# Optimization experiments

Measured on AMD Instinct MI355X. Metric: run time of the kernel, lower is better.

## Reference

```python
import jax, jax.numpy as jnp
import numpy as np
from jax import lax

B, S, I, H, O, L = 32, 512, 256, 1024, 256, 3


def setup_inputs() -> dict:
    key = jax.random.key(0)
    ks = jax.random.split(key, 10)
    sc = 0.02
    return {
        "x": jax.random.normal(ks[0], (B, S, I), dtype=jnp.float32),
        "h0": jnp.zeros((B, L, H), dtype=jnp.float32),
        # layer 0 params: gates ordered [z, r, g]
        "Wx0": jax.random.normal(ks[1], (3, H, I), dtype=jnp.float32) * sc,
        "Wh0": jax.random.normal(ks[2], (3, H, H), dtype=jnp.float32) * sc,
        "bh0": jax.random.normal(ks[3], (3, H), dtype=jnp.float32) * sc,
        # layers 1..L-1 params (input dim = H)
        "Wx": jax.random.normal(ks[4], (L - 1, 3, H, H), dtype=jnp.float32) * sc,
        "Wh": jax.random.normal(ks[5], (L - 1, 3, H, H), dtype=jnp.float32) * sc,
        "bh": jax.random.normal(ks[6], (L - 1, 3, H), dtype=jnp.float32) * sc,
        "Wout": jax.random.normal(ks[7], (O, H), dtype=jnp.float32) * sc,
        "bout": jax.random.normal(ks[8], (O,), dtype=jnp.float32) * sc,
    }


def _gru_layer(x_seq, h0, Wx, Wh, bh):
    # x_seq: [S,B,Iin], h0: [B,H], Wx: [3,H,Iin], Wh: [3,H,H], bh: [3,H]
    # Precompute all input projections once (fused GEMM over full sequence).
    xproj = jnp.einsum('sbi,ghi->sbgh', x_seq, Wx)  # [S,B,3,H]

    def step(h, xp):
        z = jax.nn.sigmoid(xp[:, 0] + h @ Wh[0].T + bh[0])
        r = jax.nn.sigmoid(xp[:, 1] + h @ Wh[1].T + bh[1])
        g = jnp.tanh(xp[:, 2] + (r * h) @ Wh[2].T + bh[2])
        h_new = z * h + (1.0 - z) * g
        return h_new, h_new

    h_last, hs = lax.scan(step, h0, xproj)
    return hs, h_last  # hs: [S,B,H]


def reference(x, h0, Wx0, Wh0, bh0, Wx, Wh, bh, Wout, bout):
    seq = jnp.transpose(x, (1, 0, 2))  # [S,B,I]
    cur, hl = _gru_layer(seq, h0[:, 0], Wx0, Wh0, bh0)
    finals = [hl]
    n_extra = Wx.shape[0]
    for i in range(n_extra):  # small fixed layer count
        cur, hl = _gru_layer(cur, h0[:, i + 1], Wx[i], Wh[i], bh[i])
        finals.append(hl)
    out = cur @ Wout.T + bout  # [S,B,O]
    layer_output = jnp.transpose(out, (1, 0, 2))  # [B,S,O]
    hidden_state = jnp.stack(finals, axis=1)  # [B,L,H]
    return layer_output, hidden_state
```

## Files before the change

### kernel.cpp

```cpp
#include <hip/hip_runtime.h>
#include <cstdint>
#include <cstddef>

#define S_  512
#define H_  1024
#define H3  3072
#define OUT_OFF 4194304

typedef __attribute__((ext_vector_type(8))) short  short8;
typedef __attribute__((ext_vector_type(4))) float  f32x4;
typedef __attribute__((ext_vector_type(4))) unsigned short us4;
typedef __attribute__((ext_vector_type(4))) unsigned int   u32x4;
typedef unsigned long long u64;

#define MFMA __builtin_amdgcn_mfma_f32_16x16x32_bf16

static const size_t XP_OFF    = 0;
static const size_t H2_OFF    = 100663296;
static const size_t XBF_OFF   = 134217728;
static const size_t WX0B_OFF  = 142606336;
static const size_t WZR0_OFF  = 144179200;
static const size_t WG0_OFF   = 148373504;
static const size_t WZR1_OFF  = 150470656;
static const size_t WGX1_OFF  = 158859264;
static const size_t WG1_OFF   = 160956416;
static const size_t WZR2_OFF  = 163053568;
static const size_t WGX2_OFF  = 171442176;
static const size_t WG2_OFF   = 173539328;
static const size_t WOUTB_OFF = 175636480;
static const size_t ZBU_OFF   = 176160768;
static const size_t GXB_OFF   = 176553984;
static const size_t HROW_OFF  = 176947200;
static const size_t FLAG_OFF  = 177340416;
static const size_t HH_OFF    = 177344512;
static const size_t RHH_OFF   = 278597632;
static const size_t WS_HIST   = 379654144;
static const size_t WS_BASE   = 177737728;

__device__ inline unsigned short f2bf(float f){
  unsigned u = __builtin_bit_cast(unsigned, f);
  unsigned r = u + 0x7fffu + ((u >> 16) & 1u);
  return (unsigned short)(r >> 16);
}
__device__ inline float bf2f(unsigned short s){
  unsigned u = ((unsigned)s) << 16;
  return __builtin_bit_cast(float, u);
}
__device__ inline unsigned ld_sys(const unsigned* p){
  return __hip_atomic_load(p, __ATOMIC_RELAXED, __HIP_MEMORY_SCOPE_AGENT);
}
__device__ inline void st_sys(unsigned* p, unsigned v){
  __hip_atomic_store(p, v, __ATOMIC_RELAXED, __HIP_MEMORY_SCOPE_AGENT);
}
__device__ inline u64 ld64(const u64* p){
  return __hip_atomic_load(p, __ATOMIC_RELAXED, __HIP_MEMORY_SCOPE_AGENT);
}
__device__ inline void st64(u64* p, u64 v){
  __hip_atomic_store(p, v, __ATOMIC_RELAXED, __HIP_MEMORY_SCOPE_AGENT);
}
template<bool HIST>
__device__ inline u64 LD(const u64* p){
  if constexpr (HIST) return *p; else return ld64(p);
}
__device__ inline short8 mk8u(u64 a, u64 b){
  u32x4 u; u.x = (unsigned)a; u.y = (unsigned)(a >> 32); u.z = (unsigned)b; u.w = (unsigned)(b >> 32);
  return __builtin_bit_cast(short8, u);
}
__device__ inline u64 pk4(float a, float b, float c, float d){
  return (u64)f2bf(a) | ((u64)f2bf(b) << 16) | ((u64)f2bf(c) << 32) | ((u64)f2bf(d) << 48);
}
__device__ inline u64 pk2f(float a, float b){
  return (u64)__builtin_bit_cast(unsigned, a) | ((u64)__builtin_bit_cast(unsigned, b) << 32);
}
__device__ inline float lo32f(u64 u){ return __builtin_bit_cast(float, (unsigned)u); }
__device__ inline float hi32f(u64 u){ return __builtin_bit_cast(float, (unsigned)(u >> 32)); }

__global__ void k_conv(const float* __restrict__ src, unsigned short* __restrict__ dst, int n){
  int i = blockIdx.x*256 + threadIdx.x;
  if (i < n) dst[i] = f2bf(src[i]);
}
__global__ void k_packzr(const float* __restrict__ Wh, const float* __restrict__ Wx,
                         unsigned short* __restrict__ dst){
  size_t i = (size_t)blockIdx.x*256 + threadIdx.x;
  int k = (int)(i & 2047);
  int n = (int)(i >> 11);
  float v = (k < 1024) ? Wh[(size_t)n*1024 + k] : Wx[(size_t)n*1024 + (k - 1024)];
  dst[i] = f2bf(v);
}
__global__ void k_convx(const float* __restrict__ x, unsigned short* __restrict__ xbf){
  int row = blockIdx.x;
  int s = row >> 5, b = row & 31;
  int i = threadIdx.x;
  xbf[(size_t)row*256 + i] = f2bf(x[((size_t)b*S_ + s)*256 + i]);
}

__global__ __launch_bounds__(256) void k_gemm(const unsigned short* __restrict__ A,
                                              const unsigned short* __restrict__ Bw,
                                              const float* __restrict__ bias,
                                              void* __restrict__ Cout,
                                              int Kd, int mode, int Nd){
  __shared__ __align__(16) unsigned short lA[128*40];
  __shared__ __align__(16) unsigned short lB[128*40];
  int bm = blockIdx.y * 128, bn = blockIdx.x * 128;
  int tid = threadIdx.x;
  int w = tid >> 6, lane = tid & 63, q = lane >> 4, cc = lane & 15;
  int wm = (w >> 1) * 64, wn = (w & 1) * 64;
  f32x4 acc[4][4] = {};
  for (int k0 = 0; k0 < Kd; k0 += 32){
    #pragma unroll
    for (int i = 0; i < 2; i++){
      int idx = tid + i*256;
      int r = idx >> 2, ch = idx & 3;
      int m = bm + r;
      int arow = (mode == 0) ? m : ((m & 511)*32 + (m >> 9));
      *(u32x4*)(lA + r*40 + ch*8) = *(const u32x4*)(A + (size_t)arow*Kd + k0 + ch*8);
      *(u32x4*)(lB + r*40 + ch*8) = *(const u32x4*)(Bw + (size_t)(bn + r)*Kd + k0 + ch*8);
    }
    __syncthreads();
    short8 af[4], bfv[4];
    #pragma unroll
    for (int i = 0; i < 4; i++) af[i]  = *(const short8*)(lA + (wm + i*16 + cc)*40 + q*8);
    #pragma unroll
    for (int i = 0; i < 4; i++) bfv[i] = *(const short8*)(lB + (wn + i*16 + cc)*40 + q*8);
    #pragma unroll
    for (int i = 0; i < 4; i++)
      #pragma unroll
      for (int j = 0; j < 4; j++)
        acc[i][j] = MFMA(af[i], bfv[j], acc[i][j], 0, 0, 0);
    __syncthreads();
  }
  if (mode == 0){
    unsigned short* xp = (unsigned short*)Cout;
    #pragma unroll
    for (int i = 0; i < 4; i++){
      #pragma unroll
      for (int j = 0; j < 4; j++){
        int m = bm + wm + i*16 + q*4;
        int n = bn + wn + j*16 + cc;
        float bv = bias[n];
        int s = m >> 5, b0 = m & 31;
        us4 pk;
        #pragma unroll
        for (int reg = 0; reg < 4; reg++) pk[reg] = f2bf(acc[i][j][reg] + bv);
        *(us4*)(xp + ((size_t)s*H3 + n)*32 + b0) = pk;
      }
    }
  } else {
    float* C = (float*)Cout;
    #pragma unroll
    for (int i = 0; i < 4; i++){
      #pragma unroll
      for (int j = 0; j < 4; j++){
        int m = bm + wm + i*16 + q*4;
        int n = bn + wn + j*16 + cc;
        float bv = bias[n];
        #pragma unroll
        for (int reg = 0; reg < 4; reg++)
          C[(size_t)(m + reg)*Nd + n] = acc[i][j][reg] + bv;
      }
    }
  }
}

__device__ inline void gbar(unsigned* flags, unsigned ep){
  __syncthreads();
  if (threadIdx.x == 0) st_sys(flags + blockIdx.x, ep);
  if (threadIdx.x < 64){
    for (;;){
      unsigned v0 = ld_sys(flags + threadIdx.x);
      unsigned v1 = ld_sys(flags + 64 + threadIdx.x);
      unsigned v2 = ld_sys(flags + 128 + threadIdx.x);
      unsigned v3 = ld_sys(flags + 192 + threadIdx.x);
      if (__all((v0 >= ep) && (v1 >= ep) && (v2 >= ep) && (v3 >= ep))) break;
      __builtin_amdgcn_s_sleep(1);
    }
  }
  __syncthreads();
}

__device__ inline void waitflags(const unsigned* f, int lo, int hi, unsigned ep){
  if (threadIdx.x < 64){
    const unsigned* p = f + lo + threadIdx.x;
    const int n = hi - lo;
    const bool h1 = (n > 64), h2 = (n > 128);
    for (;;){
      unsigned v0 = ld_sys(p);
      unsigned v1 = h1 ? ld_sys(p + 64)  : 0xffffffffu;
      unsigned v2 = h2 ? ld_sys(p + 128) : 0xffffffffu;
      if (__all((v0 >= ep) && (v1 >= ep) && (v2 >= ep))) break;
      __builtin_amdgcn_s_sleep(1);
    }
  }
  __syncthreads();
}

template<int NITER, bool HIST>
__device__ inline void matvec(const u64* p0, const unsigned short* wp,
                              f32x4& acc0, f32x4& acc1){
  u64 buf[2][4][4];
  #pragma unroll
  for (int ii = 0; ii < 4; ii++){
    const u64* p = p0 + ii*256;
    buf[0][ii][0] = LD<HIST>(p);      buf[0][ii][1] = LD<HIST>(p + 32);
    buf[0][ii][2] = LD<HIST>(p + 16); buf[0][ii][3] = LD<HIST>(p + 48);
  }
  constexpr int NCH = NITER / 4;
  #pragma unroll
  for (int ch = 0; ch < NCH; ch++){
    const int cur = ch & 1, nxt = cur ^ 1;
    if (ch + 1 < NCH){
      #pragma unroll
      for (int ii = 0; ii < 4; ii++){
        const u64* p = p0 + ((ch+1)*4 + ii)*256;
        buf[nxt][ii][0] = LD<HIST>(p);      buf[nxt][ii][1] = LD<HIST>(p + 32);
        buf[nxt][ii][2] = LD<HIST>(p + 16); buf[nxt][ii][3] = LD<HIST>(p + 48);
      }
    }
    #pragma unroll
    for (int ii = 0; ii < 4; ii++){
      short8 bw = *(const short8*)(wp + (ch*4 + ii)*32);
      acc0 = MFMA(mk8u(buf[cur][ii][0], buf[cur][ii][1]), bw, acc0, 0, 0, 0);
      acc1 = MFMA(mk8u(buf[cur][ii][2], buf[cur][ii][3]), bw, acc1, 0, 0, 0);
    }
  }
}

template<int MODE>
__global__ __launch_bounds__(256, 1) void k_fused(char* __restrict__ ws,
                                                  const float* __restrict__ h0,
                                                  const float* __restrict__ bh,
                                                  float* __restrict__ outp,
                                                  u64* __restrict__ hh,
                                                  u64* __restrict__ rhh){
  constexpr bool HIST = (MODE >= 1);
  constexpr bool DF   = (MODE == 2);

  __shared__ __align__(16) unsigned short wlds[65920];
  __shared__ __align__(16) float red[2][3][64][10];
  __shared__ float rtA[16*33];
  __shared__ float rtB[16*33];

  const int tid = threadIdx.x;
  const int w = tid >> 6, lane = tid & 63, q = (lane >> 4) & 3, c = lane & 15;
  const int i = blockIdx.x;

  const int lz   = 1 + (i >> 7);
  const int g2   = (i >> 6) & 1;
  const int n2   = (i & 63) << 4;
  const bool isl0 = (i < 128);
  const int g1   = (i >> 6) & 1;
  const int lgx  = 1 + ((i >> 6) & 1);
  const int n1   = (i & 63) << 4;
  const bool hasB = (i < 192);
  const int lb   = i >> 6;
  const int nb   = (i & 63) << 4;

  const int alo = (lb == 2) ? 128 : 0;
  const int ahi = (lb == 0) ? 128 : (lb == 1 ? 192 : 256);

  const unsigned short* xp = (const unsigned short*)(ws + XP_OFF);
  u64* h2u   = (u64*)(ws + H2_OFF);
  u64* zbu   = (u64*)(ws + ZBU_OFF);
  u64* gxb   = (u64*)(ws + GXB_OFF);
  float* hrow = (float*)(ws + HROW_OFF);
  unsigned* flags = (unsigned*)(ws + FLAG_OFF);
  unsigned* flagA = flags + 256;
  unsigned* flagB = flags + 512;

  {
    const unsigned short* src2 = (const unsigned short*)(ws + (lz == 1 ? WZR1_OFF : WZR2_OFF))
                                 + (size_t)(g2*1024 + n2)*2048;
    for (int idx = tid; idx < 4096; idx += 256){
      int kc = idx & 255, row = idx >> 8;
      u32x4 v = *(const u32x4*)(src2 + (size_t)row*2048 + kc*8);
      *(u32x4*)(wlds + row*2056 + kc*8) = v;
    }
    const unsigned short* src1 = isl0
      ? (const unsigned short*)(ws + WZR0_OFF) + (size_t)(g1*1024 + n1)*1024
      : (const unsigned short*)(ws + (lgx == 1 ? WGX1_OFF : WGX2_OFF)) + (size_t)n1*1024;
    for (int idx = tid; idx < 2048; idx += 256){
      int kc = idx & 127, row = idx >> 7;
      u32x4 v = *(const u32x4*)(src1 + (size_t)row*1024 + kc*8);
      *(u32x4*)(wlds + 32896 + row*1032 + kc*8) = v;
    }
    if (hasB){
      const unsigned short* srcb = (const unsigned short*)(ws + (lb == 0 ? WG0_OFF : (lb == 1 ? WG1_OFF : WG2_OFF)))
                                   + (size_t)nb*1024;
      for (int idx = tid; idx < 2048; idx += 256){
        int kc = idx & 127, row = idx >> 7;
        u32x4 v = *(const u32x4*)(srcb + (size_t)row*1024 + kc*8);
        *(u32x4*)(wlds + 49408 + row*1032 + kc*8) = v;
      }
    }
  }
  const float biasT2 = bh[(size_t)(lz-1)*H3 + g2*1024 + n2 + c];
  const float biasGX = isl0 ? 0.f : bh[(size_t)(lgx-1)*H3 + 2048 + n1 + c];

  if (hasB){
    for (int idx = tid; idx < 512; idx += 256){
      int n = idx >> 5, b = idx & 31;
      float v = h0[((size_t)b*3 + lb)*H_ + nb + n];
      hrow[((size_t)lb*1024 + nb + n)*32 + b] = v;
      rtA[n*33 + b] = v;
    }
  }
  __syncthreads();
  if (hasB && tid < 128){
    int b = tid & 31, p2 = tid >> 5;
    u64 pkv = pk4(rtA[(4*p2+0)*33+b], rtA[(4*p2+1)*33+b], rtA[(4*p2+2)*33+b], rtA[(4*p2+3)*33+b]);
    st64(hh + (size_t)(HIST ? lb : 0)*24576 + (size_t)lb*8192 + (size_t)((nb >> 2) + p2)*32 + b, pkv);
  }
  unsigned ep = 1;
  if constexpr (DF){
    __syncthreads();
    if (tid == 0 && hasB) st_sys(flagB + i, (unsigned)(lb + 1));
  } else {
    gbar(flags, ep); ep++;
  }

  for (int T = 0; T < 514; T++){
    const int t2 = T - lz;
    const bool actT2 = (unsigned)t2 < 512u;
    const int t1 = isl0 ? T : (T - lgx);
    const bool actT1 = (unsigned)t1 < 512u;
    const int tb = T - lb;
    const bool actB = hasB && ((unsigned)tb < 512u);

    const u64* hslotR = hh + (size_t)(HIST ? T : 0)*24576;
    u64*       rslot  = rhh + (size_t)(HIST ? T : 0)*24576;

    if constexpr (DF){
      int lo = 256, hi = 0;
      if (actT2){ int a = 64*(lz-1), b = 64*(lz+1); if (a < lo) lo = a; if (b > hi) hi = b; }
      if (actT1){
        int a = isl0 ? 0 : 64*(lgx-1);
        int b = isl0 ? 64 : 64*(lgx+1);
        if (a < lo) lo = a; if (b > hi) hi = b;
      }
      if (hi > lo) waitflags(flagB, lo, hi, (unsigned)(T + 1));
    }

    u64 hpreA[8]; us4 xpreA[2]; u64 hpreL0[8];
    if (actT2 && w == 0 && g2 == 1){
      const u64* hb = hslotR + (size_t)lz*8192 + (size_t)((n2 + c) >> 2)*32 + q*4;
      #pragma unroll
      for (int mt = 0; mt < 2; mt++)
        #pragma unroll
        for (int r = 0; r < 4; r++) hpreA[mt*4+r] = LD<HIST>(hb + mt*16 + r);
    }
    if (actT1 && w == 1 && isl0){
      const unsigned short* xr = xp + ((size_t)t1*H3 + g1*1024 + n1 + c)*32 + q*4;
      xpreA[0] = *(const us4*)(xr);
      xpreA[1] = *(const us4*)(xr + 16);
      if (g1 == 1){
        const u64* hb = hslotR + (size_t)((n1 + c) >> 2)*32 + q*4;
        #pragma unroll
        for (int mt = 0; mt < 2; mt++)
          #pragma unroll
          for (int r = 0; r < 4; r++) hpreL0[mt*4+r] = LD<HIST>(hb + mt*16 + r);
      }
    }

    f32x4 z20 = {0,0,0,0}, z21 = {0,0,0,0};
    f32x4 z10 = {0,0,0,0}, z11 = {0,0,0,0};
    if (actT2){
      const u64* p0 = hslotR + (size_t)((w < 2) ? lz : (lz-1))*8192 + (size_t)((w & 1)*128 + q*2)*32 + c;
      const unsigned short* wp = wlds + c*2056 + w*512 + q*8;
      matvec<16, HIST>(p0, wp, z20, z21);
    }
    if (actT1){
      const u64* p0 = hslotR + (size_t)(isl0 ? 0 : (lgx-1))*8192 + (size_t)(w*64 + q*2)*32 + c;
      const unsigned short* wp = wlds + 32896 + c*1032 + w*256 + q*8;
      matvec<8, HIST>(p0, wp, z10, z11);
    }
    if (actT2 && w > 0){
      float* p = &red[0][w-1][lane][0];
      #pragma unroll
      for (int r = 0; r < 4; r++){ p[r] = z20[r]; p[4+r] = z21[r]; }
    }
    if (actT1 && w != 1){
      float* p = &red[1][(w == 0) ? 0 : (w-1)][lane][0];
      #pragma unroll
      for (int r = 0; r < 4; r++){ p[r] = z10[r]; p[4+r] = z11[r]; }
    }
    __syncthreads();
    if (w == 0 && actT2){
      #pragma unroll
      for (int s = 0; s < 3; s++){
        const float* p = &red[0][s][lane][0];
        #pragma unroll
        for (int r = 0; r < 4; r++){ z20[r] += p[r]; z21[r] += p[4+r]; }
      }
      const int sh = (c & 3)*16;
      #pragma unroll
      for (int mt = 0; mt < 2; mt++){
        float f[4];
        #pragma unroll
        for (int r = 0; r < 4; r++){
          float pre = (mt ? z21[r] : z20[r]) + biasT2;
          f[r] = 1.0f / (1.0f + __expf(-pre));
        }
        if (g2 == 0){
          u64* zp = zbu + ((size_t)lz*1024 + n2 + c)*16 + mt*8 + q*2;
          st64(zp, pk2f(f[0], f[1])); st64(zp + 1, pk2f(f[2], f[3]));
        } else {
          #pragma unroll
          for (int r = 0; r < 4; r++){
            int b = mt*16 + q*4 + r;
            rtA[c*33 + b] = f[r] * bf2f((unsigned short)(hpreA[mt*4+r] >> sh));
          }
        }
      }
    }
    if (w == 1 && actT1){
      #pragma unroll
      for (int s = 0; s < 3; s++){
        const float* p = &red[1][s][lane][0];
        #pragma unroll
        for (int r = 0; r < 4; r++){ z10[r] += p[r]; z11[r] += p[4+r]; }
      }
      if (isl0){
        const int sh = (c & 3)*16;
        #pragma unroll
        for (int mt = 0; mt < 2; mt++){
          us4 xv = xpreA[mt];
          float f[4];
          #pragma unroll
          for (int r = 0; r < 4; r++){
            float pre = (mt ? z11[r] : z10[r]) + bf2f(xv[r]);
            f[r] = 1.0f / (1.0f + __expf(-pre));
          }
          if (g1 == 0){
            u64* zp = zbu + ((size_t)n1 + c)*16 + mt*8 + q*2;
            st64(zp, pk2f(f[0], f[1])); st64(zp + 1, pk2f(f[2], f[3]));
          } else {
            #pragma unroll
            for (int r = 0; r < 4; r++){
              int b = mt*16 + q*4 + r;
              rtB[c*33 + b] = f[r] * bf2f((unsigned short)(hpreL0[mt*4+r] >> sh));
            }
          }
        }
      } else {
        #pragma unroll
        for (int mt = 0; mt < 2; mt++){
          float f[4];
          #pragma unroll
          for (int r = 0; r < 4; r++) f[r] = (mt ? z11[r] : z10[r]) + biasGX;
          u64* gp = gxb + ((size_t)lgx*1024 + n1 + c)*16 + mt*8 + q*2;
          st64(gp, pk2f(f[0], f[1])); st64(gp + 1, pk2f(f[2], f[3]));
        }
      }
    }
    __syncthreads();
    if (g2 == 1 && actT2 && tid < 128){
      int b = tid & 31, p2 = tid >> 5;
      st64(rslot + (size_t)lz*8192 + (size_t)((n2 >> 2) + p2)*32 + b,
           pk4(rtA[(4*p2+0)*33+b], rtA[(4*p2+1)*33+b], rtA[(4*p2+2)*33+b], rtA[(4*p2+3)*33+b]));
    }
    if (isl0 && g1 == 1 && actT1 && tid >= 128){
      int tt = tid - 128; int b = tt & 31, p2 = tt >> 5;
      st64(rslot + (size_t)((n1 >> 2) + p2)*32 + b,
           pk4(rtB[(4*p2+0)*33+b], rtB[(4*p2+1)*33+b], rtB[(4*p2+2)*33+b], rtB[(4*p2+3)*33+b]));
    }
    if constexpr (DF){
      __syncthreads();
      if (tid == 0 && (actT2 || actT1)) st_sys(flagA + i, (unsigned)(T + 1));
      if (actB) waitflags(flagA, alo, ahi, (unsigned)(T + 1));
    } else {
      gbar(flags, ep); ep++;
    }

    u64 zpreB[4], gpreB[4]; us4 xpreB[2]; f32x4 hpre4[2];
    if (actB && w == 0){
      const u64* zp = zbu + ((size_t)lb*1024 + nb + c)*16 + q*2;
      zpreB[0] = ld64(zp);     zpreB[1] = ld64(zp + 1);
      zpreB[2] = ld64(zp + 8); zpreB[3] = ld64(zp + 9);
      if (lb == 0){
        const unsigned short* xr = xp + ((size_t)tb*H3 + 2048 + nb + c)*32 + q*4;
        xpreB[0] = *(const us4*)(xr);
        xpreB[1] = *(const us4*)(xr + 16);
      } else {
        const u64* gp = gxb + ((size_t)lb*1024 + nb + c)*16 + q*2;
        gpreB[0] = ld64(gp);     gpreB[1] = ld64(gp + 1);
        gpreB[2] = ld64(gp + 8); gpreB[3] = ld64(gp + 9);
      }
      const float* hp0 = hrow + ((size_t)lb*1024 + nb + c)*32 + q*4;
      hpre4[0] = *(const f32x4*)(hp0);
      hpre4[1] = *(const f32x4*)(hp0 + 16);
    }

    f32x4 gb0 = {0,0,0,0}, gb1 = {0,0,0,0};
    if (actB){
      const u64* p0 = (const u64*)rslot + (size_t)lb*8192 + (size_t)(w*64 + q*2)*32 + c;
      const unsigned short* wp = wlds + 49408 + c*1032 + w*256 + q*8;
      matvec<8, HIST>(p0, wp, gb0, gb1);
      if (w > 0){
        float* p = &red[0][w-1][lane][0];
        #pragma unroll
        for (int r = 0; r < 4; r++){ p[r] = gb0[r]; p[4+r] = gb1[r]; }
      }
    }
    __syncthreads();
    if (actB && w == 0){
      #pragma unroll
      for (int s = 0; s < 3; s++){
        const float* p = &red[0][s][lane][0];
        #pragma unroll
        for (int r = 0; r < 4; r++){ gb0[r] += p[r]; gb1[r] += p[4+r]; }
      }
      #pragma unroll
      for (int mt = 0; mt < 2; mt++){
        float gadd[4];
        if (lb == 0){
          us4 xv = xpreB[mt];
          #pragma unroll
          for (int r = 0; r < 4; r++) gadd[r] = bf2f(xv[r]);
        } else {
          gadd[0] = lo32f(gpreB[mt*2]);   gadd[1] = hi32f(gpreB[mt*2]);
          gadd[2] = lo32f(gpreB[mt*2+1]); gadd[3] = hi32f(gpreB[mt*2+1]);
        }
        float zf[4] = { lo32f(zpreB[mt*2]),   hi32f(zpreB[mt*2]),
                        lo32f(zpreB[mt*2+1]), hi32f(zpreB[mt*2+1]) };
        f32x4 h4 = hpre4[mt];
        f32x4 hn4;
        #pragma unroll
        for (int r = 0; r < 4; r++){
          float gpre = (mt ? gb1[r] : gb0[r]) + gadd[r];
          float gv = tanhf(gpre);
          float hnv = zf[r]*h4[r] + (1.0f - zf[r])*gv;
          hn4[r] = hnv;
          rtA[c*33 + mt*16 + q*4 + r] = hnv;
          if (tb == 511) outp[OUT_OFF + ((size_t)(mt*16 + q*4 + r)*3 + lb)*H_ + nb + c] = hnv;
        }
        *(f32x4*)(hrow + ((size_t)lb*1024 + nb + c)*32 + mt*16 + q*4) = hn4;
      }
    }
    __syncthreads();
    if (actB && tid < 128){
      int b = tid & 31, p2 = tid >> 5;
      u64 pkv = pk4(rtA[(4*p2+0)*33+b], rtA[(4*p2+1)*33+b], rtA[(4*p2+2)*33+b], rtA[(4*p2+3)*33+b]);
      st64(hh + (size_t)(HIST ? (T + 1) : 0)*24576 + (size_t)lb*8192 + (size_t)((nb >> 2) + p2)*32 + b, pkv);
      if (lb == 2) *(u64*)(h2u + ((size_t)tb*32 + b)*256 + (nb >> 2) + p2) = pkv;
    }
    if constexpr (DF){
      __syncthreads();
      if (tid == 0 && actB) st_sys(flagB + i, (unsigned)(T + 2));
    } else {
      gbar(flags, ep); ep++;
    }
  }
  (void)ep;
}

extern "C" void kernel_launch(void* const* d_in, const int* in_sizes, int n_in,
                              void* d_out, int out_size, void* d_ws, size_t ws_size,
                              hipStream_t stream){
  (void)in_sizes; (void)n_in; (void)out_size;
  if (ws_size < WS_BASE) return;
  const bool hist = (ws_size >= WS_HIST);

  const float* x    = (const float*)d_in[0];
  const float* h0   = (const float*)d_in[1];
  const float* Wx0  = (const float*)d_in[2];
  const float* Wh0  = (const float*)d_in[3];
  const float* bh0  = (const float*)d_in[4];
  const float* Wx   = (const float*)d_in[5];
  const float* Wh   = (const float*)d_in[6];
  const float* bh   = (const float*)d_in[7];
  const float* Wout = (const float*)d_in[8];
  const float* bout = (const float*)d_in[9];
  float* out = (float*)d_out;

  char* ws = (char*)d_ws;
  unsigned short* xp    = (unsigned short*)(ws + XP_OFF);
  unsigned short* h2    = (unsigned short*)(ws + H2_OFF);
  unsigned short* xbf   = (unsigned short*)(ws + XBF_OFF);
  unsigned short* wx0b  = (unsigned short*)(ws + WX0B_OFF);
  unsigned short* wzr0  = (unsigned short*)(ws + WZR0_OFF);
  unsigned short* wg0   = (unsigned short*)(ws + WG0_OFF);
  unsigned short* wzr1  = (unsigned short*)(ws + WZR1_OFF);
  unsigned short* wgx1  = (unsigned short*)(ws + WGX1_OFF);
  unsigned short* wg1   = (unsigned short*)(ws + WG1_OFF);
  unsigned short* wzr2  = (unsigned short*)(ws + WZR2_OFF);
  unsigned short* wgx2  = (unsigned short*)(ws + WGX2_OFF);
  unsigned short* wg2   = (unsigned short*)(ws + WG2_OFF);
  unsigned short* woutb = (unsigned short*)(ws + WOUTB_OFF);
  u64* hh  = (u64*)(ws + HH_OFF);
  u64* rhh = hist ? (u64*)(ws + RHH_OFF) : (hh + 24576);

  hipMemsetAsync(ws + FLAG_OFF, 0, 4096, stream);

  k_conv<<<3072, 256, 0, stream>>>(Wx0, wx0b, 786432);
  k_conv<<<8192, 256, 0, stream>>>(Wh0, wzr0, 2097152);
  k_conv<<<4096, 256, 0, stream>>>(Wh0 + 2097152, wg0, 1048576);
  k_packzr<<<16384, 256, 0, stream>>>(Wh, Wx, wzr1);
  k_conv<<<4096, 256, 0, stream>>>(Wx + 2097152, wgx1, 1048576);
  k_conv<<<4096, 256, 0, stream>>>(Wh + 2097152, wg1, 1048576);
  k_packzr<<<16384, 256, 0, stream>>>(Wh + 3145728, Wx + 3145728, wzr2);
  k_conv<<<4096, 256, 0, stream>>>(Wx + 5242880, wgx2, 1048576);
  k_conv<<<4096, 256, 0, stream>>>(Wh + 5242880, wg2, 1048576);
  k_conv<<<1024, 256, 0, stream>>>(Wout, woutb, 262144);
  k_convx<<<16384, 256, 0, stream>>>(x, xbf);

  {
    dim3 g(24, 128);
    k_gemm<<<g, 256, 0, stream>>>(xbf, wx0b, bh0, (void*)xp, 256, 0, H3);
  }
  if (hist) k_fused<2><<<256, 256, 0, stream>>>(ws, h0, bh, out, hh, rhh);
  else      k_fused<0><<<256, 256, 0, stream>>>(ws, h0, bh, out, hh, rhh);
  {
    dim3 g(2, 128);
    k_gemm<<<g, 256, 0, stream>>>(h2, woutb, bout, (void*)out, 1024, 1, 256);
  }
}
```

Before: 7.164 ms.

## Replace block-wide flag waits with per-wave polling of only the needed producer flags

```diff
diff --git a/kernel.cpp b/kernel.cpp
--- a/kernel.cpp
+++ b/kernel.cpp
@@ -178,22 +178,6 @@
   __syncthreads();
 }
 
-__device__ inline void waitflags(const unsigned* f, int lo, int hi, unsigned ep){
-  if (threadIdx.x < 64){
-    const unsigned* p = f + lo + threadIdx.x;
-    const int n = hi - lo;
-    const bool h1 = (n > 64), h2 = (n > 128);
-    for (;;){
-      unsigned v0 = ld_sys(p);
-      unsigned v1 = h1 ? ld_sys(p + 64)  : 0xffffffffu;
-      unsigned v2 = h2 ? ld_sys(p + 128) : 0xffffffffu;
-      if (__all((v0 >= ep) && (v1 >= ep) && (v2 >= ep))) break;
-      __builtin_amdgcn_s_sleep(1);
-    }
-  }
-  __syncthreads();
-}
-
 template<int NITER, bool HIST>
 __device__ inline void matvec(const u64* p0, const unsigned short* wp,
                               f32x4& acc0, f32x4& acc1){
@@ -255,9 +239,6 @@
   const int lb   = i >> 6;
   const int nb   = (i & 63) << 4;
 
-  const int alo = (lb == 2) ? 128 : 0;
-  const int ahi = (lb == 0) ? 128 : (lb == 1 ? 192 : 256);
-
   const unsigned short* xp = (const unsigned short*)(ws + XP_OFF);
   u64* h2u   = (u64*)(ws + H2_OFF);
   u64* zbu   = (u64*)(ws + ZBU_OFF);
@@ -267,6 +248,21 @@
   unsigned* flagA = flags + 256;
   unsigned* flagB = flags + 512;
 
+  int catA = (lane < 32) ? 0 : ((lane < 48) ? 1 : 2);
+  int idxA = 0;
+  if (lane < 32)      idxA = 64*((w < 2) ? lz : (lz-1)) + (w & 1)*32 + lane;
+  else if (lane < 48) idxA = 64*(isl0 ? 0 : (lgx-1)) + w*16 + (lane - 32);
+  else if (lane == 48){
+    if (w == 0){ idxA = 64*lz + (i & 63); catA = 0; }
+    else if (w == 1){ idxA = (isl0 ? 0 : 64*lgx) + (i & 63); catA = 1; }
+  }
+  const unsigned* pollA = flagB + idxA;
+  int catB = 1; int idxB = 0;
+  if (lane < 16){ idxB = ((lb == 2) ? 192 : 64) + w*16 + lane; catB = 0; }
+  else if (w == 0 && lane == 16){ idxB = ((lb == 2) ? 128 : 0) + (i & 63); catB = 0; }
+  else if (w == 0 && lane == 17 && lb >= 1){ idxB = ((lb == 1) ? 128 : 192) + (i & 63); catB = 0; }
+  const unsigned* pollB = flagA + idxB;
+
   {
     const unsigned short* src2 = (const unsigned short*)(ws + (lz == 1 ? WZR1_OFF : WZR2_OFF))
                                  + (size_t)(g2*1024 + n2)*2048;
@@ -330,14 +326,13 @@
     u64*       rslot  = rhh + (size_t)(HIST ? T : 0)*24576;
 
     if constexpr (DF){
-      int lo = 256, hi = 0;
-      if (actT2){ int a = 64*(lz-1), b = 64*(lz+1); if (a < lo) lo = a; if (b > hi) hi = b; }
-      if (actT1){
-        int a = isl0 ? 0 : 64*(lgx-1);
-        int b = isl0 ? 64 : 64*(lgx+1);
-        if (a < lo) lo = a; if (b > hi) hi = b;
-      }
-      if (hi > lo) waitflags(flagB, lo, hi, (unsigned)(T + 1));
+      const bool req = (catA == 0) ? actT2 : ((catA == 1) ? actT1 : false);
+      const unsigned epw = (unsigned)(T + 1);
+      for (;;){
+        unsigned v = req ? ld_sys(pollA) : 0xFFFFFFFFu;
+        if (__all(v >= epw)) break;
+        __builtin_amdgcn_s_sleep(2);
+      }
     }
 
     u64 hpreA[8]; us4 xpreA[2]; u64 hpreL0[8];
@@ -466,7 +461,15 @@
     if constexpr (DF){
       __syncthreads();
       if (tid == 0 && (actT2 || actT1)) st_sys(flagA + i, (unsigned)(T + 1));
-      if (actB) waitflags(flagA, alo, ahi, (unsigned)(T + 1));
+      {
+        const bool req = (catB == 0) && actB;
+        const unsigned epw = (unsigned)(T + 1);
+        for (;;){
+          unsigned v = req ? ld_sys(pollB) : 0xFFFFFFFFu;
+          if (__all(v >= epw)) break;
+          __builtin_amdgcn_s_sleep(2);
+        }
+      }
     } else {
       gbar(flags, ep); ep++;
     }
```

Result: no change. 7.225 ms (median of 2 runs) (+0.8%).
